# Kernel tuning notes

Hardware: AMD Instinct MI355X
Metric: run time of the kernel (lower is better)

The kernel has to match this reference:

```python
import jax, jax.numpy as jnp
import numpy as np
from jax import lax

B, C_IN, C_OUT, K, STYLE_DIM, H, W = 8, 512, 512, 3, 512, 64, 64


def setup_inputs() -> dict:
    key = jax.random.key(0)
    k1, k2, k3, k4 = jax.random.split(key, 4)
    return {
        "x": jax.random.normal(k1, (B, C_IN, H, W), dtype=jnp.float32),
        "style": jax.random.normal(k2, (B, STYLE_DIM), dtype=jnp.float32),
        "w": jax.random.normal(k3, (1, C_OUT, C_IN, K, K), dtype=jnp.float32),
        "affine_w": jax.random.normal(k4, (C_IN, STYLE_DIM), dtype=jnp.float32),
        "affine_b": jnp.ones((C_IN,), dtype=jnp.float32),  # bias_init=1
    }


def _per_sample_conv(xi, wi):
    # xi: [C_in, H, W], wi: [C_out, C_in, K, K]; 'same' padding, stride 1
    p = K // 2
    out = lax.conv_general_dilated(
        xi[None], wi, window_strides=(1, 1), padding=[(p, p), (p, p)],
        dimension_numbers=("NCHW", "OIHW", "NCHW"))
    return out[0]


def reference(x, style, w, affine_w, affine_b):
    # Affine (FullyConnected_Layer, linear act, lr_multiplier=1)
    weight_gain_fc = 1.0 / np.sqrt(STYLE_DIM)
    s = style @ (affine_w * weight_gain_fc).T + affine_b  # [B, C_in]

    # Modulate
    weight_gain = 1.0 / np.sqrt(C_IN * K * K)
    weight = w * weight_gain * s[:, None, :, None, None]  # [B, C_out, C_in, K, K]

    # Demodulate
    decoefs = lax.rsqrt(jnp.sum(weight * weight, axis=(2, 3, 4)) + 1e-8)  # [B, C_out]
    weight = weight * decoefs[:, :, None, None, None]

    # Per-sample conv (equivalent to groups=B grouped conv2d)
    out = jax.vmap(_per_sample_conv)(x, weight)  # [B, C_out, H, W]
    return out
```

## Files before the change

### kernel.cpp

```cpp
#include <hip/hip_runtime.h>
#include <hip/hip_bf16.h>


#define BDIM 8
#define CDIM 512
#define HW 64
#define CK 32
#define NCHUNK 16

typedef __attribute__((ext_vector_type(8))) short short8;
typedef __attribute__((ext_vector_type(4))) float float4v;

__device__ __forceinline__ short f2bf(float f) {
    unsigned u = __float_as_uint(f);
    unsigned r = (u + 0x7FFFu + ((u >> 16) & 1u)) >> 16;
    return (short)r;
}

__device__ __forceinline__ void async_ld16(const short* g, short* l) {
    __builtin_amdgcn_global_load_lds(
        (const __attribute__((address_space(1))) void*)g,
        (__attribute__((address_space(3))) void*)l, 16, 0, 0);
}


__global__ void k_affine(const float* __restrict__ style, const float* __restrict__ aw,
                         const float* __restrict__ ab, float* __restrict__ s) {
    int b = blockIdx.x;
    int ci = blockIdx.y * 256 + threadIdx.x;
    const float* st = style + b * CDIM;
    const float* w = aw + ci * CDIM;
    float acc = 0.f;
    for (int k = 0; k < CDIM; ++k) acc += st[k] * w[k];
    s[b * CDIM + ci] = acc * 0.04419417382415922f + ab[ci];
}

__global__ void k_ws2(const float* __restrict__ w, float* __restrict__ ws2) {
    int i = blockIdx.x * 256 + threadIdx.x;
    const float* p = w + i * 9;
    float a = 0.f;
#pragma unroll
    for (int t = 0; t < 9; ++t) a += p[t] * p[t];
    ws2[i] = a;
}

__global__ void k_oscale(const float* __restrict__ s, const float* __restrict__ ws2,
                         float* __restrict__ osc) {
    __shared__ float s2[CDIM];
    int b = blockIdx.x;
    int co = blockIdx.y * 256 + threadIdx.x;
    for (int i = threadIdx.x; i < CDIM; i += 256) {
        float v = s[b * CDIM + i];
        s2[i] = v * v;
    }
    __syncthreads();
    const float* r = ws2 + co * CDIM;
    float acc = 0.f;
    for (int k = 0; k < CDIM; ++k) acc += s2[k] * r[k];
    const float wg = 0.014731391274719739f;
    const float wg2 = 2.170138888888889e-4f;
    osc[b * CDIM + co] = wg * rsqrtf(wg2 * acc + 1e-8f);
}

__global__ void k_wconv(const float* __restrict__ w, short* __restrict__ wgt) {
    int idx = blockIdx.x * 256 + threadIdx.x;
    int cil = idx & 31;
    int r = idx >> 5;
    int colL = r & 127; r >>= 7;
    int t = r % 9; r /= 9;
    int ct = r & 3;
    int c = r >> 2;
    int co = ct * 128 + colL;
    int ci = c * 32 + cil;
    wgt[idx] = f2bf(w[(co * CDIM + ci) * 9 + t]);
}

__global__ __launch_bounds__(512, 2) void conv_main(
    const float* __restrict__ x, const float* __restrict__ s,
    const short* __restrict__ wgt, const float* __restrict__ osc,
    float* __restrict__ out) {

    __shared__ __align__(16) short w_lds[9 * 128 * CK];
    __shared__ __align__(16) short x_lds[2][6 * 66 * CK];

    const int tid = threadIdx.x;
    const int lane = tid & 63;
    const int wid = tid >> 6;
    const int wm = wid >> 2;
    const int wn = wid & 3;
    const int l15 = lane & 15;
    const int l4 = lane >> 4;

    const int bx = blockIdx.x;
    const int xcd = bx & 7;
    const int ct = (bx >> 3) & 3;
    const int gh = bx >> 5;
    const int g = gh * 8 + xcd;
    const int b = g & 7;
    const int rt = g >> 3;
    const int r0 = rt * 4;

    const int cig = lane & 3;
    const int col = wn * 16 + (lane >> 2);

    for (int i = tid; i < 768; i += 512) {
        int bufi = i >= 384;
        int rem = i - bufi * 384;
        int rr = rem >> 6;
        int rem2 = rem & 63;
        int cc = (rem2 >= 32) ? 65 : 0;
        int cidx = rem2 & 31;
        x_lds[bufi][(rr * 66 + cc) * CK + cidx] = 0;
    }

    float rx[24];
    float sv[8];

    auto stage_w = [&](int c) {
        const short* src = wgt + (c * 4 + ct) * (9 * 128 * CK);
#pragma unroll
        for (int k = 0; k < 9; ++k) {
            int off = (k * 512 + wid * 64) * 8;
            async_ld16(src + off + lane * 8, w_lds + off);
        }
    };

    auto stage_x_load = [&](int c) {
#pragma unroll
        for (int j = 0; j < 8; ++j) sv[j] = s[b * CDIM + c * 32 + cig * 8 + j];
#pragma unroll
        for (int i = 0; i < 3; ++i) {
            int row = wm + i * 2;
            int grow = r0 - 1 + row;
            bool ok = (grow >= 0) && (grow < HW);
            int growc = ok ? grow : 0;
            const float* base = x + ((b * CDIM + c * 32 + cig * 8) * HW + growc) * HW + col;
#pragma unroll
            for (int j = 0; j < 8; ++j) {
                float v = base[j * (HW * HW)];
                rx[i * 8 + j] = ok ? v : 0.0f;
            }
        }
    };

    auto stage_x_write = [&](int buf) {
        int lcol = 1 + col;
        int qs = (cig ^ (lcol & 3)) * 8;
#pragma unroll
        for (int i = 0; i < 3; ++i) {
            int row = wm + i * 2;
            short8 pk;
#pragma unroll
            for (int j = 0; j < 8; ++j) pk[j] = f2bf(rx[i * 8 + j] * sv[j]);
            *(short8*)&x_lds[buf][(row * 66 + lcol) * CK + qs] = pk;
        }
    };

    float4v acc[4][4] = {};

    auto compute = [&](int buf) {
        const short* xb = x_lds[buf];
#pragma unroll
        for (int dh = -1; dh <= 1; ++dh) {
            int lrow = wn + dh + 1;
#pragma unroll
            for (int dw = -1; dw <= 1; ++dw) {
                int t = (dh + 1) * 3 + (dw + 1);
                short8 a[4], bf[4];
#pragma unroll
                for (int mf = 0; mf < 4; ++mf)
                    a[mf] = *(const short8*)&w_lds[(t * 128 + wm * 64 + mf * 16 + l15) * CK + l4 * 8];
                int cb = 1 + dw + l15;
                int xq = (l4 ^ (cb & 3)) * 8;
#pragma unroll
                for (int nf = 0; nf < 4; ++nf)
                    bf[nf] = *(const short8*)&xb[(lrow * 66 + cb + nf * 16) * CK + xq];
#pragma unroll
                for (int mf = 0; mf < 4; ++mf)
#pragma unroll
                    for (int nf = 0; nf < 4; ++nf)
                        acc[mf][nf] = __builtin_amdgcn_mfma_f32_16x16x32_bf16(
                            a[mf], bf[nf], acc[mf][nf], 0, 0, 0);
            }
        }
    };

    stage_w(0);
    stage_x_load(0);
    stage_x_write(0);
    __syncthreads();

    int cur = 0;
    for (int c = 0; c < NCHUNK; ++c) {
        if (c + 1 < NCHUNK) stage_x_load(c + 1);
        compute(cur);
        if (c + 1 < NCHUNK) {
            __syncthreads();
            stage_w(c + 1);
            stage_x_write(cur ^ 1);
            __syncthreads();
            cur ^= 1;
        }
    }

    const int row_out = r0 + wn;
#pragma unroll
    for (int mf = 0; mf < 4; ++mf) {
#pragma unroll
        for (int j = 0; j < 4; ++j) {
            int co = ct * 128 + wm * 64 + mf * 16 + l4 * 4 + j;
            float oscv = osc[b * CDIM + co];
            float* po = out + ((b * CDIM + co) * HW + row_out) * HW;
#pragma unroll
            for (int nf = 0; nf < 4; ++nf)
                po[nf * 16 + l15] = acc[mf][nf][j] * oscv;
        }
    }
}


extern "C" void kernel_launch(void* const* d_in, const int* in_sizes, int n_in,
                              void* d_out, int out_size, void* d_ws, size_t ws_size,
                              hipStream_t stream) {
    const float* x     = (const float*)d_in[0];
    const float* style = (const float*)d_in[1];
    const float* w     = (const float*)d_in[2];
    const float* aw    = (const float*)d_in[3];
    const float* ab    = (const float*)d_in[4];
    float* out = (float*)d_out;

    float* s_buf = (float*)d_ws;
    float* ws2   = s_buf + 4096;
    float* osc   = ws2 + 262144;
    short* wgt   = (short*)(osc + 4096);

    k_affine<<<dim3(8, 2), 256, 0, stream>>>(style, aw, ab, s_buf);
    k_ws2<<<1024, 256, 0, stream>>>(w, ws2);
    k_wconv<<<9216, 256, 0, stream>>>(w, wgt);
    k_oscale<<<dim3(8, 2), 256, 0, stream>>>(s_buf, ws2, osc);
    conv_main<<<512, 512, 0, stream>>>(x, s_buf, wgt, osc, out);
}
```

Measured before the change: 188.1 us.

## Enlarge conv tile to 8 output rows per block with fragment-ordered weights

Each block now covers 128 output channels by 8 output rows, and each wave computes a full 128x64 row tile (8x4 MFMA fragments), so the grid halves to 256 blocks. Weights are pre-permuted into the exact MFMA A-fragment lane order, which makes LDS weight reads contiguous per lane. The x swizzle and the block-to-batch mapping are also changed. The aim is to cut halo reloads of x, reuse each B fragment across 8 weight fragments, and lower LDS traffic per MFMA. In exchange, register pressure doubles (acc[8][4]) and there are fewer blocks per CU to hide latency.

```diff
diff --git a/kernel.cpp b/kernel.cpp
--- a/kernel.cpp
+++ b/kernel.cpp
@@ -2,7 +2,6 @@
 #include <hip/hip_bf16.h>
 
 
-#define BDIM 8
 #define CDIM 512
 #define HW 64
 #define CK 32
@@ -64,14 +63,20 @@
 
 __global__ void k_wconv(const float* __restrict__ w, short* __restrict__ wgt) {
     int idx = blockIdx.x * 256 + threadIdx.x;
-    int cil = idx & 31;
-    int r = idx >> 5;
-    int colL = r & 127; r >>= 7;
-    int t = r % 9; r /= 9;
-    int ct = r & 3;
-    int c = r >> 2;
-    int co = ct * 128 + colL;
-    int ci = c * 32 + cil;
+    int j = idx & 7;
+    int slotg = idx >> 3;
+    int region = slotg / 4608;
+    int a16 = slotg - region * 4608;
+    int tm = a16 >> 6;
+    int t = tm >> 3;
+    int mf = tm & 7;
+    int sl = a16 & 63;
+    int l4 = sl >> 4;
+    int l15 = sl & 15;
+    int ct = region & 3;
+    int c = region >> 2;
+    int co = ct * 128 + mf * 16 + l15;
+    int ci = c * 32 + l4 * 8 + j;
     wgt[idx] = f2bf(w[(co * CDIM + ci) * 9 + t]);
 }
 
@@ -80,44 +85,42 @@
     const short* __restrict__ wgt, const float* __restrict__ osc,
     float* __restrict__ out) {
 
-    __shared__ __align__(16) short w_lds[9 * 128 * CK];
-    __shared__ __align__(16) short x_lds[2][6 * 66 * CK];
+    __shared__ __align__(16) short w_lds[9 * 8 * 64 * 8];
+    __shared__ __align__(16) short x_lds[2][10 * 66 * CK];
 
     const int tid = threadIdx.x;
     const int lane = tid & 63;
     const int wid = tid >> 6;
-    const int wm = wid >> 2;
-    const int wn = wid & 3;
     const int l15 = lane & 15;
     const int l4 = lane >> 4;
 
     const int bx = blockIdx.x;
-    const int xcd = bx & 7;
-    const int ct = (bx >> 3) & 3;
-    const int gh = bx >> 5;
-    const int g = gh * 8 + xcd;
-    const int b = g & 7;
-    const int rt = g >> 3;
-    const int r0 = rt * 4;
-
-    const int cig = lane & 3;
-    const int col = wn * 16 + (lane >> 2);
-
-    for (int i = tid; i < 768; i += 512) {
-        int bufi = i >= 384;
-        int rem = i - bufi * 384;
-        int rr = rem >> 6;
-        int rem2 = rem & 63;
-        int cc = (rem2 >= 32) ? 65 : 0;
-        int cidx = rem2 & 31;
-        x_lds[bufi][(rr * 66 + cc) * CK + cidx] = 0;
-    }
-
-    float rx[24];
-    float sv[8];
+    const int ct = (bx >> 1) & 3;
+    const int bpar = bx & 1;
+    const int rest = bx >> 3;
+    const int b = 2 * (rest & 3) + bpar;
+    const int rt = rest >> 2;
+    const int r0 = rt * 8;
+
+    const int cig = tid & 3;
+    const int col = (tid >> 2) & 63;
+    const int rowhalf = tid >> 8;
+
+    for (int i = tid; i < 640; i += 512) {
+        int bufi = i >= 320;
+        int v = i - bufi * 320;
+        int row = v >> 5;
+        int w16 = v & 31;
+        int colh = (w16 >= 16) ? 65 : 0;
+        int q16 = w16 & 15;
+        ((unsigned*)x_lds[bufi])[(row * 66 + colh) * 16 + q16] = 0u;
+    }
+
+    float rx[40];
+    float4v sva, svb;
 
     auto stage_w = [&](int c) {
-        const short* src = wgt + (c * 4 + ct) * (9 * 128 * CK);
+        const short* src = wgt + (c * 4 + ct) * 36864;
 #pragma unroll
         for (int k = 0; k < 9; ++k) {
             int off = (k * 512 + wid * 64) * 8;
@@ -126,15 +129,14 @@
     };
 
     auto stage_x_load = [&](int c) {
-#pragma unroll
-        for (int j = 0; j < 8; ++j) sv[j] = s[b * CDIM + c * 32 + cig * 8 + j];
-#pragma unroll
-        for (int i = 0; i < 3; ++i) {
-            int row = wm + i * 2;
+        const float4v* sp = (const float4v*)&s[b * CDIM + c * 32 + cig * 8];
+        sva = sp[0]; svb = sp[1];
+#pragma unroll
+        for (int i = 0; i < 5; ++i) {
+            int row = 2 * i + rowhalf;
             int grow = r0 - 1 + row;
             bool ok = (grow >= 0) && (grow < HW);
-            int growc = ok ? grow : 0;
-            const float* base = x + ((b * CDIM + c * 32 + cig * 8) * HW + growc) * HW + col;
+            const float* base = x + ((b * CDIM + c * 32 + cig * 8) * HW + (ok ? grow : 0)) * HW + col;
 #pragma unroll
             for (int j = 0; j < 8; ++j) {
                 float v = base[j * (HW * HW)];
@@ -144,43 +146,44 @@
     };
 
     auto stage_x_write = [&](int buf) {
-        int lcol = 1 + col;
-        int qs = (cig ^ (lcol & 3)) * 8;
-#pragma unroll
-        for (int i = 0; i < 3; ++i) {
-            int row = wm + i * 2;
+        int lcol = col + 1;
+        int q = cig ^ ((lcol >> 1) & 3);
+#pragma unroll
+        for (int i = 0; i < 5; ++i) {
+            int row = 2 * i + rowhalf;
             short8 pk;
 #pragma unroll
-            for (int j = 0; j < 8; ++j) pk[j] = f2bf(rx[i * 8 + j] * sv[j]);
-            *(short8*)&x_lds[buf][(row * 66 + lcol) * CK + qs] = pk;
-        }
-    };
-
-    float4v acc[4][4] = {};
+            for (int j = 0; j < 8; ++j) {
+                float sj = (j < 4) ? sva[j] : svb[j - 4];
+                pk[j] = f2bf(rx[i * 8 + j] * sj);
+            }
+            *(short8*)&x_lds[buf][(row * 66 + lcol) * CK + q * 8] = pk;
+        }
+    };
+
+    float4v acc[8][4] = {};
 
     auto compute = [&](int buf) {
         const short* xb = x_lds[buf];
 #pragma unroll
-        for (int dh = -1; dh <= 1; ++dh) {
-            int lrow = wn + dh + 1;
-#pragma unroll
-            for (int dw = -1; dw <= 1; ++dw) {
-                int t = (dh + 1) * 3 + (dw + 1);
-                short8 a[4], bf[4];
-#pragma unroll
-                for (int mf = 0; mf < 4; ++mf)
-                    a[mf] = *(const short8*)&w_lds[(t * 128 + wm * 64 + mf * 16 + l15) * CK + l4 * 8];
-                int cb = 1 + dw + l15;
-                int xq = (l4 ^ (cb & 3)) * 8;
+        for (int t = 0; t < 9; ++t) {
+            int dh = t / 3 - 1;
+            int dw = t % 3 - 1;
+            int lrow = wid + dh + 1;
+            short8 bfr[4];
+#pragma unroll
+            for (int nf = 0; nf < 4; ++nf) {
+                int lcol = 1 + nf * 16 + l15 + dw;
+                int xq = l4 ^ ((lcol >> 1) & 3);
+                bfr[nf] = *(const short8*)&xb[(lrow * 66 + lcol) * CK + xq * 8];
+            }
+#pragma unroll
+            for (int mf = 0; mf < 8; ++mf) {
+                short8 af = *(const short8*)&w_lds[((t * 8 + mf) * 64 + lane) * 8];
 #pragma unroll
                 for (int nf = 0; nf < 4; ++nf)
-                    bf[nf] = *(const short8*)&xb[(lrow * 66 + cb + nf * 16) * CK + xq];
-#pragma unroll
-                for (int mf = 0; mf < 4; ++mf)
-#pragma unroll
-                    for (int nf = 0; nf < 4; ++nf)
-                        acc[mf][nf] = __builtin_amdgcn_mfma_f32_16x16x32_bf16(
-                            a[mf], bf[nf], acc[mf][nf], 0, 0, 0);
+                    acc[mf][nf] = __builtin_amdgcn_mfma_f32_16x16x32_bf16(
+                        af, bfr[nf], acc[mf][nf], 0, 0, 0);
             }
         }
     };
@@ -191,6 +194,7 @@
     __syncthreads();
 
     int cur = 0;
+#pragma unroll 1
     for (int c = 0; c < NCHUNK; ++c) {
         if (c + 1 < NCHUNK) stage_x_load(c + 1);
         compute(cur);
@@ -203,17 +207,17 @@
         }
     }
 
-    const int row_out = r0 + wn;
-#pragma unroll
-    for (int mf = 0; mf < 4; ++mf) {
+    const int row_out = r0 + wid;
+#pragma unroll
+    for (int mf = 0; mf < 8; ++mf) {
+        float4v ov = *(const float4v*)&osc[b * CDIM + ct * 128 + mf * 16 + l4 * 4];
 #pragma unroll
         for (int j = 0; j < 4; ++j) {
-            int co = ct * 128 + wm * 64 + mf * 16 + l4 * 4 + j;
-            float oscv = osc[b * CDIM + co];
+            int co = ct * 128 + mf * 16 + l4 * 4 + j;
             float* po = out + ((b * CDIM + co) * HW + row_out) * HW;
 #pragma unroll
             for (int nf = 0; nf < 4; ++nf)
-                po[nf * 16 + l15] = acc[mf][nf][j] * oscv;
+                po[nf * 16 + l15] = acc[mf][nf][j] * ov[j];
         }
     }
 }
@@ -238,5 +242,5 @@
     k_ws2<<<1024, 256, 0, stream>>>(w, ws2);
     k_wconv<<<9216, 256, 0, stream>>>(w, wgt);
     k_oscale<<<dim3(8, 2), 256, 0, stream>>>(s_buf, ws2, osc);
-    conv_main<<<512, 512, 0, stream>>>(x, s_buf, wgt, osc, out);
-}
+    conv_main<<<256, 512, 0, stream>>>(x, s_buf, wgt, osc, out);
+}
```

Measured after the change: 205.8 us. 1.09x slower.
